# Optimization experiments

Hardware: AMD Instinct MI355X
Metric: run time of the kernel (lower is better)

The kernel has to match this reference:

```python
import jax, jax.numpy as jnp
import numpy as np

WINDOW_SIZE = 9
EPS = 1e-05


def _box_sum(x, w):
    """Zero-padded 3D box-filter sum, computed separably (one 1D conv per axis).
    Identical math to conv3d with an all-ones [w,w,w] kernel and zero padding."""
    pad = w // 2
    dn = ('NCDHW', 'OIDHW', 'NCDHW')
    for ax in range(3):  # D, H, W
        kshape = [1, 1, 1, 1, 1]
        kshape[2 + ax] = w
        kernel = jnp.ones(kshape, x.dtype)
        padding = [(0, 0)] * 3
        padding[ax] = (pad, pad)
        x = jax.lax.conv_general_dilated(x, kernel, (1, 1, 1), padding,
                                         dimension_numbers=dn)
    return x


def setup_inputs() -> dict:
    key = jax.random.key(0)
    k1, k2 = jax.random.split(key)
    shape = (2, 1, 160, 160, 160)
    predicted = jax.random.uniform(k1, shape, dtype=jnp.float32)
    target = jax.random.uniform(k2, shape, dtype=jnp.float32)
    return {"predicted": predicted, "target": target}


def reference(predicted, target):
    I = predicted.astype(jnp.float32)
    J = target.astype(jnp.float32)
    w = WINDOW_SIZE
    win_size = jnp.float32(w ** 3)

    I_sum = _box_sum(I, w)
    J_sum = _box_sum(J, w)
    I2_sum = _box_sum(I * I, w)
    J2_sum = _box_sum(J * J, w)
    IJ_sum = _box_sum(I * J, w)

    u_I = I_sum / win_size
    u_J = J_sum / win_size

    cross = IJ_sum - u_J * I_sum - u_I * J_sum + u_I * u_J * win_size
    I_var = I2_sum - 2.0 * u_I * I_sum + u_I * u_I * win_size
    J_var = J2_sum - 2.0 * u_J * J_sum + u_J * u_J * win_size

    cc = cross * cross / (I_var * J_var + EPS)
    cc = jnp.clip(cc, 0.0, 1.0)
    return 1.0 - jnp.mean(cc)
```

## Files before the change

kernel.cpp:

```cpp
#include <hip/hip_runtime.h>
#include <hip/hip_fp16.h>


#define DIM 160
#define HW  (160 * 160)
#define VOL (160 * 160 * 160)
#define NBATCH 2
#define TH 8
#define SR 16
#define THB 320
#define SEG 10
#define NSEG (DIM / SEG)

struct __align__(16) h8 { __half2 a, b, c, d; };
struct __align__(8) h4 { __half2 a, b; };
typedef float v2f __attribute__((ext_vector_type(2)));

__device__ inline float4 dec8(unsigned int u) {
    v2f lo = __builtin_amdgcn_cvt_pk_f32_fp8((int)u, false);
    v2f hi = __builtin_amdgcn_cvt_pk_f32_fp8((int)u, true);
    return make_float4(lo[0], lo[1], hi[0], hi[1]);
}

__device__ inline unsigned int enc8(float a, float b, float c, float d) {
    int u = __builtin_amdgcn_cvt_pk_fp8_f32(a, b, 0, false);
    u = __builtin_amdgcn_cvt_pk_fp8_f32(c, d, u, true);
    return (unsigned int)u;
}

__global__ __launch_bounds__(THB) void k1_boxsum2d(const float* __restrict__ I,
                                                   const float* __restrict__ J,
                                                   unsigned char* __restrict__ A8) {
    __shared__ __half wsl[5][SR][DIM];

    const int tid = threadIdx.x;
    const int orig = blockIdx.x;
    const int wgid = (orig & 7) * 800 + (orig >> 3);
    const int ty = wgid % 20;
    const int rest = wgid / 20;
    const int d = rest % DIM;
    const int batch = rest / DIM;
    const int h0 = ty * TH;
    const float* Ib = I + (size_t)batch * VOL + (size_t)d * HW;
    const float* Jb = J + (size_t)batch * VOL + (size_t)d * HW;

    {
        const int r = tid / 20, g = tid % 20;
        const int gh = h0 - 4 + r;
        const int gw = 8 * g - 4;
        __half* wrow = &wsl[0][0][0] + (r * DIM + 8 * g);

        if (gh < 0 || gh >= DIM) {
            const __half2 hz = __float2half2_rn(0.f);
            h8 z; z.a = hz; z.b = hz; z.c = hz; z.d = hz;
#pragma unroll
            for (int ch = 0; ch < 5; ++ch)
                *(h8*)(wrow + ch * (SR * DIM)) = z;
        } else {
            const float* pI = Ib + gh * DIM;
            const float* pJ = Jb + gh * DIM;
            float a[16], b[16];
#pragma unroll
            for (int q = 0; q < 4; ++q) {
                int c0 = gw + 4 * q;
                if (c0 >= 0 && c0 < DIM) {
                    *(float4*)&a[4 * q] = *(const float4*)(pI + c0);
                    *(float4*)&b[4 * q] = *(const float4*)(pJ + c0);
                } else {
                    *(float4*)&a[4 * q] = make_float4(0.f, 0.f, 0.f, 0.f);
                    *(float4*)&b[4 * q] = make_float4(0.f, 0.f, 0.f, 0.f);
                }
            }
#define PROC(CH, VAL)                                                       \
            {                                                               \
                float o[8];                                                 \
                float ss = 0.f;                                             \
                _Pragma("unroll")                                           \
                for (int k = 0; k < 9; ++k) { ss += (VAL); }                \
                o[0] = ss;                                                  \
                _Pragma("unroll")                                           \
                for (int j = 1; j < 8; ++j) {                               \
                    int k = j + 8; float add_ = (VAL);                      \
                    k = j - 1;     float sub_ = (VAL);                      \
                    ss += add_ - sub_;                                      \
                    o[j] = ss;                                              \
                }                                                           \
                h8 v;                                                       \
                v.a = __floats2half2_rn(o[0], o[1]);                        \
                v.b = __floats2half2_rn(o[2], o[3]);                        \
                v.c = __floats2half2_rn(o[4], o[5]);                        \
                v.d = __floats2half2_rn(o[6], o[7]);                        \
                *(h8*)(wrow + CH * (SR * DIM)) = v;                         \
            }
            PROC(0, a[k])
            PROC(1, b[k])
            PROC(2, a[k] * a[k])
            PROC(3, b[k] * b[k])
            PROC(4, a[k] * b[k])
#undef PROC
        }
    }
    __syncthreads();

    {
        const int q = tid % 40, r8 = tid / 40;
        const int wp0 = 2 * q;
        const size_t ob = (size_t)batch * 5 * VOL + (size_t)d * HW +
                          (size_t)(h0 + r8) * DIM + 4 * q;
#pragma unroll
        for (int ch = 0; ch < 5; ++ch) {
            const __half2* col = (const __half2*)&wsl[ch][r8][0] + wp0;
            h4 v = *(const h4*)col;
            __half2 sa = v.a, sb = v.b;
#pragma unroll
            for (int k = 1; k < 9; ++k) {
                h4 u = *(const h4*)(col + k * (DIM / 2));
                sa = __hadd2(sa, u.a);
                sb = __hadd2(sb, u.b);
            }
            float2 f0 = __half22float2(sa);
            float2 f1 = __half22float2(sb);
            *(unsigned int*)(A8 + ob + (size_t)ch * VOL) =
                enc8(f0.x, f0.y, f1.x, f1.y);
        }
    }
}

__device__ inline void cc_accum(float s0, float s1, float s2, float s3,
                                float s4, float& acc) {
    const float inv_wsz = 1.0f / 729.0f;
    float cross = s4 - s0 * s1 * inv_wsz;
    float Ivar  = s2 - s0 * s0 * inv_wsz;
    float Jvar  = s3 - s1 * s1 * inv_wsz;
    float cc = cross * cross * __builtin_amdgcn_rcpf(Ivar * Jvar + 1e-5f);
    acc += fminf(fmaxf(cc, 0.0f), 1.0f);
}

__global__ __launch_bounds__(256) void k2_dsum_final(const unsigned char* __restrict__ A8,
                                                     float* __restrict__ partial) {
    const int batch = blockIdx.y;
    const unsigned int* B = (const unsigned int*)(A8 + (size_t)batch * 5 * VOL);
    const int PLW = VOL / 4;
    const int HWW = HW / 4;
    int t = blockIdx.x * 256 + threadIdx.x;
    int wq = t % 40;
    int rest = t / 40;
    int h = rest % DIM;
    int seg = rest / DIM;
    int d0 = seg * SEG;
    const int base = h * 40 + wq;

    float4 s0 = {0,0,0,0}, s1 = {0,0,0,0}, s2 = {0,0,0,0},
           s3 = {0,0,0,0}, s4 = {0,0,0,0};
#define ACC4(sv, ch, idx, sgn)                                              \
    {                                                                       \
        float4 v_ = dec8(B[(ch) * PLW + (idx)]);                            \
        sv.x sgn v_.x; sv.y sgn v_.y; sv.z sgn v_.z; sv.w sgn v_.w;         \
    }
#pragma unroll
    for (int k = -4; k <= 4; ++k) {
        int dd = d0 + k;
        if (dd >= 0) {
            int idx = base + dd * HWW;
            ACC4(s0, 0, idx, +=) ACC4(s1, 1, idx, +=) ACC4(s2, 2, idx, +=)
            ACC4(s3, 3, idx, +=) ACC4(s4, 4, idx, +=)
        }
    }

    float acc = 0.f;
    for (int d = d0; d < d0 + SEG; ++d) {
        cc_accum(s0.x, s1.x, s2.x, s3.x, s4.x, acc);
        cc_accum(s0.y, s1.y, s2.y, s3.y, s4.y, acc);
        cc_accum(s0.z, s1.z, s2.z, s3.z, s4.z, acc);
        cc_accum(s0.w, s1.w, s2.w, s3.w, s4.w, acc);
        int lead = d + 5, trail = d - 4;
        if (lead < DIM) {
            int li = base + lead * HWW;
            ACC4(s0, 0, li, +=) ACC4(s1, 1, li, +=) ACC4(s2, 2, li, +=)
            ACC4(s3, 3, li, +=) ACC4(s4, 4, li, +=)
        }
        if (trail >= 0) {
            int ti = base + trail * HWW;
            ACC4(s0, 0, ti, -=) ACC4(s1, 1, ti, -=) ACC4(s2, 2, ti, -=)
            ACC4(s3, 3, ti, -=) ACC4(s4, 4, ti, -=)
        }
    }
#undef ACC4

#pragma unroll
    for (int off = 32; off > 0; off >>= 1) acc += __shfl_down(acc, off);
    __shared__ float ws4[4];
    if ((threadIdx.x & 63) == 0) ws4[threadIdx.x >> 6] = acc;
    __syncthreads();
    if (threadIdx.x == 0)
        partial[batch * 400 + blockIdx.x] = ws4[0] + ws4[1] + ws4[2] + ws4[3];
}

__global__ __launch_bounds__(256) void final_reduce(const float* __restrict__ partial,
                                                    int n, float* __restrict__ out) {
    float a = 0.f;
    for (int i = threadIdx.x; i < n; i += 256) a += partial[i];
#pragma unroll
    for (int off = 32; off > 0; off >>= 1) a += __shfl_down(a, off);
    __shared__ float ws4[4];
    if ((threadIdx.x & 63) == 0) ws4[threadIdx.x >> 6] = a;
    __syncthreads();
    if (threadIdx.x == 0)
        out[0] = 1.0f - (ws4[0] + ws4[1] + ws4[2] + ws4[3]) *
                            (1.0f / (float)(NBATCH * VOL));
}

extern "C" void kernel_launch(void* const* d_in, const int* in_sizes, int n_in,
                              void* d_out, int out_size, void* d_ws, size_t ws_size,
                              hipStream_t stream) {
    const float* I = (const float*)d_in[0];
    const float* J = (const float*)d_in[1];
    float* out = (float*)d_out;

    unsigned char* A8 = (unsigned char*)d_ws;
    float* partial = (float*)(A8 + (size_t)NBATCH * 5 * VOL);

    k1_boxsum2d<<<20 * DIM * NBATCH, THB, 0, stream>>>(I, J, A8);
    dim3 g2(400, NBATCH);
    k2_dsum_final<<<g2, 256, 0, stream>>>(A8, partial);
    final_reduce<<<1, 256, 0, stream>>>(partial, NBATCH * 400, out);
}
```

Before: 53.92 us.

## Double row tile height and use sliding-window H sums in first kernel

Each block in the 2D box-sum kernel now covers 16 output rows instead of 8, so the halo rows loaded per output row drop from 8/16 to 8/24. The H-direction sum now computes 4 consecutive output rows per thread with a running sliding window (subtract the outgoing row, add the incoming one) instead of a full 9-tap sum per row. Stores become 2-byte fp8 pairs rather than 4-byte words. The tradeoff is fewer blocks, a second load-loop iteration for some threads, narrower global stores, and fp16 rounding error that builds up through the running sums.

```diff
diff --git a/kernel.cpp b/kernel.cpp
--- a/kernel.cpp
+++ b/kernel.cpp
@@ -6,14 +6,13 @@
 #define HW  (160 * 160)
 #define VOL (160 * 160 * 160)
 #define NBATCH 2
-#define TH 8
-#define SR 16
+#define TH 16
+#define SR 24
 #define THB 320
 #define SEG 10
 #define NSEG (DIM / SEG)
 
 struct __align__(16) h8 { __half2 a, b, c, d; };
-struct __align__(8) h4 { __half2 a, b; };
 typedef float v2f __attribute__((ext_vector_type(2)));
 
 __device__ inline float4 dec8(unsigned int u) {
@@ -22,10 +21,8 @@
     return make_float4(lo[0], lo[1], hi[0], hi[1]);
 }
 
-__device__ inline unsigned int enc8(float a, float b, float c, float d) {
-    int u = __builtin_amdgcn_cvt_pk_fp8_f32(a, b, 0, false);
-    u = __builtin_amdgcn_cvt_pk_fp8_f32(c, d, u, true);
-    return (unsigned int)u;
+__device__ inline unsigned short enc2(float a, float b) {
+    return (unsigned short)(__builtin_amdgcn_cvt_pk_fp8_f32(a, b, 0, false) & 0xffff);
 }
 
 __global__ __launch_bounds__(THB) void k1_boxsum2d(const float* __restrict__ I,
@@ -35,17 +32,17 @@
 
     const int tid = threadIdx.x;
     const int orig = blockIdx.x;
-    const int wgid = (orig & 7) * 800 + (orig >> 3);
-    const int ty = wgid % 20;
-    const int rest = wgid / 20;
+    const int wgid = (orig & 7) * 400 + (orig >> 3);
+    const int ty = wgid % 10;
+    const int rest = wgid / 10;
     const int d = rest % DIM;
     const int batch = rest / DIM;
     const int h0 = ty * TH;
     const float* Ib = I + (size_t)batch * VOL + (size_t)d * HW;
     const float* Jb = J + (size_t)batch * VOL + (size_t)d * HW;
 
-    {
-        const int r = tid / 20, g = tid % 20;
+    for (int t = tid; t < 480; t += THB) {
+        const int r = t / 20, g = t % 20;
         const int gh = h0 - 4 + r;
         const int gw = 8 * g - 4;
         __half* wrow = &wsl[0][0][0] + (r * DIM + 8 * g);
@@ -103,25 +100,30 @@
     __syncthreads();
 
     {
-        const int q = tid % 40, r8 = tid / 40;
-        const int wp0 = 2 * q;
-        const size_t ob = (size_t)batch * 5 * VOL + (size_t)d * HW +
-                          (size_t)(h0 + r8) * DIM + 4 * q;
+        const int wp = tid % 80;
+        const int rq = tid / 80;
+        const size_t obase = (size_t)batch * 5 * VOL + (size_t)d * HW +
+                             (size_t)(h0 + 4 * rq) * DIM + 2 * wp;
 #pragma unroll
         for (int ch = 0; ch < 5; ++ch) {
-            const __half2* col = (const __half2*)&wsl[ch][r8][0] + wp0;
-            h4 v = *(const h4*)col;
-            __half2 sa = v.a, sb = v.b;
-#pragma unroll
-            for (int k = 1; k < 9; ++k) {
-                h4 u = *(const h4*)(col + k * (DIM / 2));
-                sa = __hadd2(sa, u.a);
-                sb = __hadd2(sb, u.b);
-            }
-            float2 f0 = __half22float2(sa);
-            float2 f1 = __half22float2(sb);
-            *(unsigned int*)(A8 + ob + (size_t)ch * VOL) =
-                enc8(f0.x, f0.y, f1.x, f1.y);
+            const __half2* col = (const __half2*)&wsl[ch][4 * rq][0] + wp;
+            __half2 c[12];
+#pragma unroll
+            for (int k = 0; k < 12; ++k) c[k] = col[k * (DIM / 2)];
+            __half2 s = c[0];
+#pragma unroll
+            for (int k = 1; k < 9; ++k) s = __hadd2(s, c[k]);
+            unsigned char* Ao = A8 + obase + (size_t)ch * VOL;
+            {
+                float2 f = __half22float2(s);
+                *(unsigned short*)Ao = enc2(f.x, f.y);
+            }
+#pragma unroll
+            for (int j = 1; j < 4; ++j) {
+                s = __hadd2(__hsub2(s, c[j - 1]), c[j + 8]);
+                float2 f = __half22float2(s);
+                *(unsigned short*)(Ao + (size_t)j * DIM) = enc2(f.x, f.y);
+            }
         }
     }
 }
@@ -220,7 +222,7 @@
     unsigned char* A8 = (unsigned char*)d_ws;
     float* partial = (float*)(A8 + (size_t)NBATCH * 5 * VOL);
 
-    k1_boxsum2d<<<20 * DIM * NBATCH, THB, 0, stream>>>(I, J, A8);
+    k1_boxsum2d<<<(DIM / TH) * DIM * NBATCH, THB, 0, stream>>>(I, J, A8);
     dim3 g2(400, NBATCH);
     k2_dsum_final<<<g2, 256, 0, stream>>>(A8, partial);
     final_reduce<<<1, 256, 0, stream>>>(partial, NBATCH * 400, out);
```

Result: slower. 56.59 us (+5.0%).

## Process two depth slices per block and prefetch the second during the H pass

Applied to the files above, without the earlier changes.

Each k1 workgroup now handles two consecutive D slices instead of one, halving the grid. The global loads for the second slice are issued before the H-direction pass of the first slice, so memory latency overlaps with LDS compute. The cost is more registers for the extra row buffers, which may lower occupancy, plus an extra barrier per block.

```diff
diff --git a/kernel.cpp b/kernel.cpp
--- a/kernel.cpp
+++ b/kernel.cpp
@@ -35,95 +35,118 @@
 
     const int tid = threadIdx.x;
     const int orig = blockIdx.x;
-    const int wgid = (orig & 7) * 800 + (orig >> 3);
+    const int wgid = (orig & 7) * 400 + (orig >> 3);
     const int ty = wgid % 20;
     const int rest = wgid / 20;
-    const int d = rest % DIM;
-    const int batch = rest / DIM;
+    const int dz = rest % 80;
+    const int batch = rest / 80;
     const int h0 = ty * TH;
-    const float* Ib = I + (size_t)batch * VOL + (size_t)d * HW;
-    const float* Jb = J + (size_t)batch * VOL + (size_t)d * HW;
-
-    {
-        const int r = tid / 20, g = tid % 20;
-        const int gh = h0 - 4 + r;
-        const int gw = 8 * g - 4;
-        __half* wrow = &wsl[0][0][0] + (r * DIM + 8 * g);
-
-        if (gh < 0 || gh >= DIM) {
-            const __half2 hz = __float2half2_rn(0.f);
-            h8 z; z.a = hz; z.b = hz; z.c = hz; z.d = hz;
-#pragma unroll
-            for (int ch = 0; ch < 5; ++ch)
-                *(h8*)(wrow + ch * (SR * DIM)) = z;
-        } else {
-            const float* pI = Ib + gh * DIM;
-            const float* pJ = Jb + gh * DIM;
-            float a[16], b[16];
-#pragma unroll
-            for (int q = 0; q < 4; ++q) {
-                int c0 = gw + 4 * q;
-                if (c0 >= 0 && c0 < DIM) {
-                    *(float4*)&a[4 * q] = *(const float4*)(pI + c0);
-                    *(float4*)&b[4 * q] = *(const float4*)(pJ + c0);
-                } else {
-                    *(float4*)&a[4 * q] = make_float4(0.f, 0.f, 0.f, 0.f);
-                    *(float4*)&b[4 * q] = make_float4(0.f, 0.f, 0.f, 0.f);
-                }
-            }
-#define PROC(CH, VAL)                                                       \
-            {                                                               \
-                float o[8];                                                 \
-                float ss = 0.f;                                             \
-                _Pragma("unroll")                                           \
-                for (int k = 0; k < 9; ++k) { ss += (VAL); }                \
-                o[0] = ss;                                                  \
-                _Pragma("unroll")                                           \
-                for (int j = 1; j < 8; ++j) {                               \
-                    int k = j + 8; float add_ = (VAL);                      \
-                    k = j - 1;     float sub_ = (VAL);                      \
-                    ss += add_ - sub_;                                      \
-                    o[j] = ss;                                              \
-                }                                                           \
-                h8 v;                                                       \
-                v.a = __floats2half2_rn(o[0], o[1]);                        \
-                v.b = __floats2half2_rn(o[2], o[3]);                        \
-                v.c = __floats2half2_rn(o[4], o[5]);                        \
-                v.d = __floats2half2_rn(o[6], o[7]);                        \
-                *(h8*)(wrow + CH * (SR * DIM)) = v;                         \
-            }
-            PROC(0, a[k])
-            PROC(1, b[k])
-            PROC(2, a[k] * a[k])
-            PROC(3, b[k] * b[k])
-            PROC(4, a[k] * b[k])
+    const int d0 = 2 * dz;
+    const float* Ib = I + (size_t)batch * VOL;
+    const float* Jb = J + (size_t)batch * VOL;
+
+    const int r = tid / 20, g = tid % 20;
+    const int gh = h0 - 4 + r;
+    const int gw = 8 * g - 4;
+    const bool rowok = (gh >= 0) && (gh < DIM);
+
+    float a[16], b[16], a2[16], b2[16];
+
+#define LOADROW(d, A_, B_)                                                  \
+    if (rowok) {                                                            \
+        const float* pI = Ib + (size_t)(d) * HW + gh * DIM;                 \
+        const float* pJ = Jb + (size_t)(d) * HW + gh * DIM;                 \
+        _Pragma("unroll")                                                   \
+        for (int q = 0; q < 4; ++q) {                                       \
+            int c0 = gw + 4 * q;    \
+            if (c0 >= 0 && c0 < DIM) {                                      \
+                *(float4*)&A_[4 * q] = *(const float4*)(pI + c0);           \
+                *(float4*)&B_[4 * q] = *(const float4*)(pJ + c0);           \
+            } else {                                                        \
+                *(float4*)&A_[4 * q] = make_float4(0.f, 0.f, 0.f, 0.f);     \
+                *(float4*)&B_[4 * q] = make_float4(0.f, 0.f, 0.f, 0.f);     \
+            }                                                               \
+        }                                                                   \
+    }
+
+#define WSTAGE(A_, B_)                                                      \
+    {                                                                       \
+        __half* wrow = &wsl[0][0][0] + (r * DIM + 8 * g);                   \
+        if (!rowok) {                                                       \
+            const __half2 hz = __float2half2_rn(0.f);                       \
+            h8 z; z.a = hz; z.b = hz; z.c = hz; z.d = hz;                   \
+            _Pragma("unroll")                                               \
+            for (int ch = 0; ch < 5; ++ch)                                  \
+                *(h8*)(wrow + ch * (SR * DIM)) = z;                         \
+        } else {                                                            \
+            PROC(0, A_[k], wrow)                                            \
+            PROC(1, B_[k], wrow)                                            \
+            PROC(2, A_[k] * A_[k], wrow)                                    \
+            PROC(3, B_[k] * B_[k], wrow)                                    \
+            PROC(4, A_[k] * B_[k], wrow)                                    \
+        }                                                                   \
+    }
+
+#define PROC(CH, VAL, WROW)                                                 \
+    {                                                                       \
+        float o[8];                                                         \
+        float ss = 0.f;                                                     \
+        _Pragma("unroll")                                                   \
+        for (int k = 0; k < 9; ++k) { ss += (VAL); }                        \
+        o[0] = ss;                                                          \
+        _Pragma("unroll")                                                   \
+        for (int j = 1; j < 8; ++j) {                                       \
+            int k = j + 8; float add_ = (VAL);                              \
+            k = j - 1;     float sub_ = (VAL);                              \
+            ss += add_ - sub_;                                              \
+            o[j] = ss;                                                      \
+        }                                                                   \
+        h8 v;                                                               \
+        v.a = __floats2half2_rn(o[0], o[1]);                                \
+        v.b = __floats2half2_rn(o[2], o[3]);                                \
+        v.c = __floats2half2_rn(o[4], o[5]);                                \
+        v.d = __floats2half2_rn(o[6], o[7]);                                \
+        *(h8*)(WROW + CH * (SR * DIM)) = v;                                 \
+    }
+
+#define HSTAGE(d)                                                           \
+    {                                                                       \
+        const int q = tid % 40, r8 = tid / 40;                              \
+        const int wp0 = 2 * q;                                              \
+        const size_t ob = (size_t)batch * 5 * VOL + (size_t)(d) * HW +      \
+                          (size_t)(h0 + r8) * DIM + 4 * q;                  \
+        _Pragma("unroll")                                                   \
+        for (int ch = 0; ch < 5; ++ch) {                                    \
+            const __half2* col = (const __half2*)&wsl[ch][r8][0] + wp0;     \
+            h4 v = *(const h4*)col;                                         \
+            __half2 sa = v.a, sb = v.b;                                     \
+            _Pragma("unroll")                                               \
+            for (int k = 1; k < 9; ++k) {                                   \
+                h4 u = *(const h4*)(col + k * (DIM / 2));                   \
+                sa = __hadd2(sa, u.a);                                      \
+                sb = __hadd2(sb, u.b);                                      \
+            }                                                               \
+            float2 f0 = __half22float2(sa);                                 \
+            float2 f1 = __half22float2(sb);                                 \
+            *(unsigned int*)(A8 + ob + (size_t)ch * VOL) =                  \
+                enc8(f0.x, f0.y, f1.x, f1.y);                               \
+        }                                                                   \
+    }
+
+    LOADROW(d0, a, b)
+    WSTAGE(a, b)
+    __syncthreads();
+    LOADROW(d0 + 1, a2, b2)
+    HSTAGE(d0)
+    __syncthreads();
+    WSTAGE(a2, b2)
+    __syncthreads();
+    HSTAGE(d0 + 1)
+
+#undef LOADROW
+#undef WSTAGE
 #undef PROC
-        }
-    }
-    __syncthreads();
-
-    {
-        const int q = tid % 40, r8 = tid / 40;
-        const int wp0 = 2 * q;
-        const size_t ob = (size_t)batch * 5 * VOL + (size_t)d * HW +
-                          (size_t)(h0 + r8) * DIM + 4 * q;
-#pragma unroll
-        for (int ch = 0; ch < 5; ++ch) {
-            const __half2* col = (const __half2*)&wsl[ch][r8][0] + wp0;
-            h4 v = *(const h4*)col;
-            __half2 sa = v.a, sb = v.b;
-#pragma unroll
-            for (int k = 1; k < 9; ++k) {
-                h4 u = *(const h4*)(col + k * (DIM / 2));
-                sa = __hadd2(sa, u.a);
-                sb = __hadd2(sb, u.b);
-            }
-            float2 f0 = __half22float2(sa);
-            float2 f1 = __half22float2(sb);
-            *(unsigned int*)(A8 + ob + (size_t)ch * VOL) =
-                enc8(f0.x, f0.y, f1.x, f1.y);
-        }
-    }
+#undef HSTAGE
 }
 
 __device__ inline void cc_accum(float s0, float s1, float s2, float s3,
@@ -220,7 +243,7 @@
     unsigned char* A8 = (unsigned char*)d_ws;
     float* partial = (float*)(A8 + (size_t)NBATCH * 5 * VOL);
 
-    k1_boxsum2d<<<20 * DIM * NBATCH, THB, 0, stream>>>(I, J, A8);
+    k1_boxsum2d<<<20 * 80 * NBATCH, THB, 0, stream>>>(I, J, A8);
     dim3 g2(400, NBATCH);
     k2_dsum_final<<<g2, 256, 0, stream>>>(A8, partial);
     final_reduce<<<1, 256, 0, stream>>>(partial, NBATCH * 400, out);
```

Measured after the change: 55.60 us. 1.03x slower.
